# Performance work log

Measured on AMD Instinct MI355X. Metric: run time of the kernel, lower is better.

The kernel has to match this reference:

```python
import jax, jax.numpy as jnp
import numpy as np

N_HEADS = 2


def setup_inputs() -> dict:
    key = jax.random.key(0)
    ks = jax.random.split(key, 12)
    B, S, d, g = 4096, 32, 512, 512
    sp = (1.0 / np.sqrt(d))
    sg = (1.0 / np.sqrt(g))
    return {
        "source": jax.random.normal(ks[0], (B, d), jnp.float32),
        "gene": jax.random.normal(ks[1], (B, S, g), jnp.float32),
        "neighbors_padding_mask": jax.random.bernoulli(ks[2], 0.3, (B, S)),
        "mask_n": jax.random.uniform(ks[3], (B, 1), jnp.float32),
        "Wq": jax.random.normal(ks[4], (d, d), jnp.float32) * sp,
        "bq": jax.random.normal(ks[5], (d,), jnp.float32) * 0.02,
        "Wk": jax.random.normal(ks[6], (d, g), jnp.float32) * sg,
        "bk": jax.random.normal(ks[7], (d,), jnp.float32) * 0.02,
        "Wv": jax.random.normal(ks[8], (d, g), jnp.float32) * sg,
        "bv": jax.random.normal(ks[9], (d,), jnp.float32) * 0.02,
        "Wout": jax.random.normal(ks[10], (d, d), jnp.float32) * sp,
        "bout": jax.random.normal(ks[11], (d,), jnp.float32) * 0.02,
    }


def reference(source, gene, neighbors_padding_mask, mask_n,
              Wq, bq, Wk, bk, Wv, bv, Wout, bout):
    # attention_node.forward: 1-query masked MHA over S temporal neighbors.
    B, S, _ = gene.shape
    d = source.shape[1]
    H = N_HEADS
    hd = d // H

    # rows where every neighbor is padded -> unmask slot 0 (torch in-place fix)
    invalid = jnp.all(neighbors_padding_mask, axis=1, keepdims=True)      # [B,1]
    mask = neighbors_padding_mask.at[:, 0].set(
        jnp.where(invalid[:, 0], False, neighbors_padding_mask[:, 0]))

    # separate q/k/v projections (kdim=vdim=n_gene != embed_dim)
    q = (source @ Wq.T + bq) * (hd ** -0.5)                               # [B,d]
    k = gene @ Wk.T + bk                                                  # [B,S,d]
    v = gene @ Wv.T + bv                                                  # [B,S,d]

    qh = q.reshape(B, H, hd)
    kh = k.reshape(B, S, H, hd)
    vh = v.reshape(B, S, H, hd)

    scores = jnp.einsum('bhd,bshd->bhs', qh, kh)                          # [B,H,S]
    scores = jnp.where(mask[:, None, :], -jnp.inf, scores)
    w = jax.nn.softmax(scores, axis=-1)                                   # [B,H,S]

    attn = jnp.einsum('bhs,bshd->bhd', w, vh).reshape(B, d)               # [B,d]
    attn_out = attn @ Wout.T + bout

    # zero rows with no valid neighbors, gate, residual
    attn_out = jnp.where(invalid, jnp.float32(0), attn_out)
    out = attn_out * mask_n + source                                      # [B,d]
    attn_weight = w.mean(axis=1)                                          # avg over heads, [B,S]
    return out, attn_weight
```

## Files before the change

### kernel.cpp

```cpp
#include <hip/hip_runtime.h>
#include <hip/hip_bf16.h>
#include <math.h>
#include <stdint.h>


#define NB 4096
#define SNB 32
#define DM 512

typedef __attribute__((ext_vector_type(8))) short bf16x8;
typedef __attribute__((ext_vector_type(4))) float f32x4;

__device__ __forceinline__ unsigned short f2bf(float f) {
    union { float f; unsigned int u; } v; v.f = f;
    unsigned int u = v.u;
    return (unsigned short)((u + 0x7FFFu + ((u >> 16) & 1u)) >> 16);
}
__device__ __forceinline__ float bf2f(unsigned short s) {
    union { unsigned int u; float f; } v; v.u = ((unsigned int)s) << 16;
    return v.f;
}

__global__ __launch_bounds__(256) void k_prep(
    const float* __restrict__ src, const float* __restrict__ Wq,
    const float* __restrict__ bq, const float* __restrict__ Wk,
    const float* __restrict__ Wv, const float* __restrict__ Wout,
    const float* __restrict__ bv, const float* __restrict__ bout,
    const unsigned int* __restrict__ maskw,
    unsigned short* __restrict__ srcb, unsigned short* __restrict__ WkT,
    unsigned short* __restrict__ WqT, unsigned short* __restrict__ WvT,
    unsigned short* __restrict__ WoutB,
    float* __restrict__ cb, float* __restrict__ e, int* __restrict__ mode)
{
    __shared__ float tile[32][33];
    __shared__ int fF, fH;
    int bid = blockIdx.x, t = threadIdx.x;

    if (bid == 0) {
        if (t == 0) { fF = 0; fH = 0; }
        __syncthreads();
        int lf = 0, lh = 0;
        for (int i = t; i < 32768; i += 256) {
            unsigned int w = maskw[i];
            lf |= (w == 0x3F800000u);
            lh |= ((w & 0xFFFFFF00u) != 0u);
        }
        if (lf) atomicOr(&fF, 1);
        if (lh) atomicOr(&fH, 1);
        __syncthreads();
        if (t == 0) *mode = fF ? 2 : (fH ? 1 : 0);
        return;
    }
    if (bid <= 4) {
        int idx = (bid - 1) * 256 + t;
        int h = idx >> 9, j = idx & 511;
        float a = 0.f;
        for (int i = 0; i < 256; i++)
            a += Wk[(size_t)(h * 256 + i) * 512 + j] * bq[h * 256 + i];
        cb[idx] = 0.0625f * a;
        return;
    }
    if (bid <= 6) {
        int n = (bid - 5) * 256 + t;
        const float4* wr = (const float4*)(Wout + (size_t)n * 512);
        const float4* bv4 = (const float4*)bv;
        float a = bout[n];
        for (int q = 0; q < 128; q++) {
            float4 wv = wr[q], vv = bv4[q];
            a += wv.x * vv.x + wv.y * vv.y + wv.z * vv.z + wv.w * vv.w;
        }
        e[n] = a;
        return;
    }
    if (bid < 775) {
        const float* sm; unsigned short* dst; float scale; int tt;
        if (bid < 263)      { tt = bid - 7;   sm = Wk; dst = WkT; scale = 0.0625f; }
        else if (bid < 519) { tt = bid - 263; sm = Wv; dst = WvT; scale = 1.0f; }
        else                { tt = bid - 519; sm = Wq; dst = WqT; scale = 1.0f; }
        int i0 = (tt >> 4) << 5, j0 = (tt & 15) << 5;
        int r = t >> 3, c4 = (t & 7) << 2;
        float4 v = *(const float4*)(sm + (size_t)(i0 + r) * 512 + j0 + c4);
        tile[r][c4 + 0] = v.x; tile[r][c4 + 1] = v.y;
        tile[r][c4 + 2] = v.z; tile[r][c4 + 3] = v.w;
        __syncthreads();
        int jj = t >> 3, ig = (t & 7) << 2;
        int h = i0 >> 8, ib = i0 & 255;
        ushort4 o;
        o.x = f2bf(tile[ig + 0][jj] * scale);
        o.y = f2bf(tile[ig + 1][jj] * scale);
        o.z = f2bf(tile[ig + 2][jj] * scale);
        o.w = f2bf(tile[ig + 3][jj] * scale);
        *(ushort4*)(dst + (size_t)h * 131072 + (size_t)(j0 + jj) * 256 + ib + ig) = o;
        return;
    }
    if (bid < 807) {
        int base = (bid - 775) * 2048;
        for (int q = 0; q < 8; q++) {
            int idx = base + q * 256 + t;
            float4 v = ((const float4*)Wout)[idx];
            ushort4 o;
            o.x = f2bf(v.x); o.y = f2bf(v.y); o.z = f2bf(v.z); o.w = f2bf(v.w);
            ((ushort4*)WoutB)[idx] = o;
        }
        return;
    }
    {
        int base = (bid - 807) * 2048;
        for (int q = 0; q < 8; q++) {
            int idx = base + q * 256 + t;
            float4 v = ((const float4*)src)[idx];
            ushort4 o;
            o.x = f2bf(v.x); o.y = f2bf(v.y); o.z = f2bf(v.z); o.w = f2bf(v.w);
            ((ushort4*)srcb)[idx] = o;
        }
    }
}

__global__ __launch_bounds__(256) void k_cd(
    const unsigned short* __restrict__ WkT, const unsigned short* __restrict__ WqT,
    const unsigned short* __restrict__ WoutB, const unsigned short* __restrict__ WvT,
    unsigned short* __restrict__ C, unsigned short* __restrict__ D)
{
    __shared__ __align__(16) unsigned short As[64 * 40];
    __shared__ __align__(16) unsigned short Bs[64 * 40];
    int bid = blockIdx.x, t = threadIdx.x;
    const unsigned short *A, *Bt;
    unsigned short* outp;
    int lda, ldb, ldo;
    if (bid < 128) {
        int m0 = (bid >> 3) << 6, n0 = (bid & 7) << 6, h = m0 >> 9;
        A = WkT + (size_t)m0 * 256; lda = 256;
        Bt = WqT + (size_t)h * 131072 + (size_t)n0 * 256; ldb = 256;
        outp = C + (size_t)m0 * 512 + n0; ldo = 512;
    } else {
        int b2 = bid - 128;
        int m0 = (b2 >> 4) << 6, n0 = (b2 & 15) << 6, h = n0 >> 9;
        A = WoutB + (size_t)m0 * 512 + h * 256; lda = 512;
        Bt = WvT + (size_t)n0 * 256; ldb = 256;
        outp = D + (size_t)m0 * 1024 + n0; ldo = 1024;
    }
    int w = t >> 6, l = t & 63;
    int wm = (w >> 1) << 5, wn = (w & 1) << 5;
    int quad = l >> 4, lm = l & 15;
    f32x4 acc00 = {0.f,0.f,0.f,0.f}, acc01 = {0.f,0.f,0.f,0.f};
    f32x4 acc10 = {0.f,0.f,0.f,0.f}, acc11 = {0.f,0.f,0.f,0.f};
    int srow = t >> 2, spart = t & 3;
    const unsigned short* ag = A + (size_t)srow * lda + spart * 8;
    const unsigned short* bg = Bt + (size_t)srow * ldb + spart * 8;
    unsigned short* asl = As + srow * 40 + spart * 8;
    unsigned short* bsl = Bs + srow * 40 + spart * 8;
    for (int k0 = 0; k0 < 256; k0 += 32) {
        *(bf16x8*)asl = *(const bf16x8*)ag;
        *(bf16x8*)bsl = *(const bf16x8*)bg;
        ag += 32; bg += 32;
        __syncthreads();
        bf16x8 a0 = *(const bf16x8*)(As + (wm + lm) * 40 + quad * 8);
        bf16x8 a1 = *(const bf16x8*)(As + (wm + 16 + lm) * 40 + quad * 8);
        bf16x8 b0 = *(const bf16x8*)(Bs + (wn + lm) * 40 + quad * 8);
        bf16x8 b1 = *(const bf16x8*)(Bs + (wn + 16 + lm) * 40 + quad * 8);
        acc00 = __builtin_amdgcn_mfma_f32_16x16x32_bf16(a0, b0, acc00, 0, 0, 0);
        acc01 = __builtin_amdgcn_mfma_f32_16x16x32_bf16(a0, b1, acc01, 0, 0, 0);
        acc10 = __builtin_amdgcn_mfma_f32_16x16x32_bf16(a1, b0, acc10, 0, 0, 0);
        acc11 = __builtin_amdgcn_mfma_f32_16x16x32_bf16(a1, b1, acc11, 0, 0, 0);
        __syncthreads();
    }
    f32x4 accs[2][2] = {{acc00, acc01}, {acc10, acc11}};
    for (int ms = 0; ms < 2; ms++)
        for (int ns = 0; ns < 2; ns++)
            for (int r = 0; r < 4; r++)
                outp[(size_t)(wm + ms * 16 + quad * 4 + r) * ldo + wn + ns * 16 + lm] =
                    f2bf(accs[ms][ns][r]);
}

template <int EPI>
__global__ __launch_bounds__(256) void k_gemm_bt(
    const unsigned short* __restrict__ A, const unsigned short* __restrict__ Bt,
    void* __restrict__ outp, const float* __restrict__ bias,
    const float* __restrict__ gscale, const float* __restrict__ resid,
    int M, int N, int K)
{
    __shared__ __align__(16) unsigned short As[64 * 40];
    __shared__ __align__(16) unsigned short Bs[64 * 40];
    int nt = N >> 6;
    int m0 = ((int)blockIdx.x / nt) << 6;
    int n0 = ((int)blockIdx.x % nt) << 6;
    int t = threadIdx.x;
    int w = t >> 6, l = t & 63;
    int wm = (w >> 1) << 5, wn = (w & 1) << 5;
    int quad = l >> 4, lm = l & 15;

    f32x4 acc00 = {0.f,0.f,0.f,0.f}, acc01 = {0.f,0.f,0.f,0.f};
    f32x4 acc10 = {0.f,0.f,0.f,0.f}, acc11 = {0.f,0.f,0.f,0.f};

    int srow = t >> 2, spart = t & 3;
    const unsigned short* ag = A + (size_t)(m0 + srow) * K + spart * 8;
    const unsigned short* bg = Bt + (size_t)(n0 + srow) * K + spart * 8;
    unsigned short* asl = As + srow * 40 + spart * 8;
    unsigned short* bsl = Bs + srow * 40 + spart * 8;

    for (int k0 = 0; k0 < K; k0 += 32) {
        *(bf16x8*)asl = *(const bf16x8*)ag;
        *(bf16x8*)bsl = *(const bf16x8*)bg;
        ag += 32; bg += 32;
        __syncthreads();
        bf16x8 a0 = *(const bf16x8*)(As + (wm + lm) * 40 + quad * 8);
        bf16x8 a1 = *(const bf16x8*)(As + (wm + 16 + lm) * 40 + quad * 8);
        bf16x8 b0 = *(const bf16x8*)(Bs + (wn + lm) * 40 + quad * 8);
        bf16x8 b1 = *(const bf16x8*)(Bs + (wn + 16 + lm) * 40 + quad * 8);
        acc00 = __builtin_amdgcn_mfma_f32_16x16x32_bf16(a0, b0, acc00, 0, 0, 0);
        acc01 = __builtin_amdgcn_mfma_f32_16x16x32_bf16(a0, b1, acc01, 0, 0, 0);
        acc10 = __builtin_amdgcn_mfma_f32_16x16x32_bf16(a1, b0, acc10, 0, 0, 0);
        acc11 = __builtin_amdgcn_mfma_f32_16x16x32_bf16(a1, b1, acc11, 0, 0, 0);
        __syncthreads();
    }
    f32x4 accs[2][2] = {{acc00, acc01}, {acc10, acc11}};
    for (int ms = 0; ms < 2; ms++) {
        for (int ns = 0; ns < 2; ns++) {
            int n = n0 + wn + ns * 16 + lm;
            float bval = bias[n];
            for (int r = 0; r < 4; r++) {
                int m = m0 + wm + ms * 16 + quad * 4 + r;
                float v = accs[ms][ns][r] + bval;
                if (EPI == 0) {
                    ((unsigned short*)outp)[(size_t)m * N + n] = f2bf(v);
                } else {
                    ((float*)outp)[(size_t)m * N + n] =
                        v * gscale[m] + resid[(size_t)m * N + n];
                }
            }
        }
    }
}

__global__ __launch_bounds__(256) void k_attn(
    const float* __restrict__ gene, const unsigned short* __restrict__ QKb,
    const void* __restrict__ maskbuf, const int* __restrict__ modep,
    const float* __restrict__ mask_n,
    unsigned short* __restrict__ G, float* __restrict__ gscale,
    float* __restrict__ aw_out)
{
    __shared__ __align__(16) unsigned short glb[32 * 520];
    __shared__ __align__(16) float sp[4 * 64];
    __shared__ __align__(16) float wls[64];
    __shared__ int msk_s[32];

    int b = blockIdx.x, t = threadIdx.x;
    int w = t >> 6, l = t & 63, quad = l >> 4, lm = l & 15;

    bf16x8 af[4];
    {
        const unsigned short* qp = QKb + (size_t)b * 1024 + (size_t)lm * 512
                                 + w * 128 + quad * 8;
#pragma unroll
        for (int kk = 0; kk < 4; kk++) {
            bf16x8 z = {0,0,0,0,0,0,0,0};
            af[kk] = (lm < 2) ? *(const bf16x8*)(qp + kk * 32) : z;
        }
    }

    const float4* gp = (const float4*)(gene + (size_t)b * (SNB * DM));
    for (int it = 0; it < 8; it++) {
        float4 v0 = gp[t * 2 + it * 512];
        float4 v1 = gp[t * 2 + 1 + it * 512];
        int s = (t >> 6) + it * 4;
        int col = (t & 63) * 8;
        bf16x8 pk;
        pk[0] = (short)f2bf(v0.x); pk[1] = (short)f2bf(v0.y);
        pk[2] = (short)f2bf(v0.z); pk[3] = (short)f2bf(v0.w);
        pk[4] = (short)f2bf(v1.x); pk[5] = (short)f2bf(v1.y);
        pk[6] = (short)f2bf(v1.z); pk[7] = (short)f2bf(v1.w);
        *(bf16x8*)(glb + s * 520 + col) = pk;
    }
    int mode = *modep;
    if (t < 32) {
        size_t moff = (size_t)b * 32 + t;
        int mv;
        if (mode == 1)      mv = ((const unsigned char*)maskbuf)[moff] != 0;
        else if (mode == 2) mv = (((const float*)maskbuf)[moff] != 0.0f);
        else                mv = (((const int*)maskbuf)[moff] != 0);
        msk_s[t] = mv;
    }
    __syncthreads();

    if (t == 0) {
        int all = 1;
        for (int s = 0; s < 32; s++) all &= msk_s[s];
        if (all) msk_s[0] = 0;
        gscale[b] = all ? 0.0f : mask_n[b];
    }

    {
        f32x4 s0 = {0.f,0.f,0.f,0.f}, s1 = {0.f,0.f,0.f,0.f};
        int kb = w * 128;
#pragma unroll
        for (int kk = 0; kk < 4; kk++) {
            int k0 = kb + kk * 32;
            bf16x8 b0 = *(const bf16x8*)(glb + lm * 520 + k0 + quad * 8);
            bf16x8 b1 = *(const bf16x8*)(glb + (16 + lm) * 520 + k0 + quad * 8);
            s0 = __builtin_amdgcn_mfma_f32_16x16x32_bf16(af[kk], b0, s0, 0, 0, 0);
            s1 = __builtin_amdgcn_mfma_f32_16x16x32_bf16(af[kk], b1, s1, 0, 0, 0);
        }
        if (quad == 0) {
            sp[w * 64 + lm] = s0[0];
            sp[w * 64 + 32 + lm] = s0[1];
            sp[w * 64 + 16 + lm] = s1[0];
            sp[w * 64 + 48 + lm] = s1[1];
        }
    }
    __syncthreads();

    if (t < 64) {
        int s = t & 31;
        float v = sp[t] + sp[64 + t] + sp[128 + t] + sp[192 + t];
        int mk = msk_s[s];
        float vm = mk ? -1e30f : v;
        for (int off = 16; off > 0; off >>= 1) vm = fmaxf(vm, __shfl_xor(vm, off, 64));
        float ex = mk ? 0.0f : __expf(v - vm);
        float sm = ex;
        for (int off = 16; off > 0; off >>= 1) sm += __shfl_xor(sm, off, 64);
        wls[t] = ex / sm;
    }
    __syncthreads();

    if (t < 32) aw_out[(size_t)b * 32 + t] = 0.5f * (wls[t] + wls[32 + t]);

    {
        int h = t >> 7, jg = (t & 127) << 2;
        float a0 = 0.f, a1 = 0.f, a2 = 0.f, a3 = 0.f;
        const float* wrow = wls + h * 32;
        for (int s4 = 0; s4 < 8; s4++) {
            float4 wv = *(const float4*)(wrow + s4 * 4);
#pragma unroll
            for (int si = 0; si < 4; si++) {
                int s = s4 * 4 + si;
                ushort4 gv = *(const ushort4*)(glb + s * 520 + jg);
                float wq = (si == 0) ? wv.x : (si == 1) ? wv.y : (si == 2) ? wv.z : wv.w;
                a0 += wq * bf2f(gv.x); a1 += wq * bf2f(gv.y);
                a2 += wq * bf2f(gv.z); a3 += wq * bf2f(gv.w);
            }
        }
        ushort4 ov;
        ov.x = f2bf(a0); ov.y = f2bf(a1); ov.z = f2bf(a2); ov.w = f2bf(a3);
        *(ushort4*)(G + (size_t)b * 1024 + h * 512 + jg) = ov;
    }
}

extern "C" void kernel_launch(void* const* d_in, const int* in_sizes, int n_in,
                              void* d_out, int out_size, void* d_ws, size_t ws_size,
                              hipStream_t stream)
{
    const float* src   = (const float*)d_in[0];
    const float* gene  = (const float*)d_in[1];
    const void*  mask  = d_in[2];
    const float* maskn = (const float*)d_in[3];
    const float* Wq    = (const float*)d_in[4];
    const float* bq    = (const float*)d_in[5];
    const float* Wk    = (const float*)d_in[6];
    const float* Wv    = (const float*)d_in[8];
    const float* bv    = (const float*)d_in[9];
    const float* Wout  = (const float*)d_in[10];
    const float* bout  = (const float*)d_in[11];

    float* out = (float*)d_out;
    float* aw  = out + (size_t)NB * DM;

    char* ws = (char*)d_ws;
    size_t off = 0;
    auto alloc = [&](size_t bytes) -> void* {
        void* p = ws + off;
        off = (off + bytes + 255) & ~((size_t)255);
        return p;
    };
    int* mode            = (int*)alloc(4);
    unsigned short* srcb = (unsigned short*)alloc((size_t)NB * DM * 2);
    unsigned short* WkT  = (unsigned short*)alloc((size_t)1024 * 256 * 2);
    unsigned short* WqT  = (unsigned short*)alloc((size_t)1024 * 256 * 2);
    unsigned short* WvT  = (unsigned short*)alloc((size_t)1024 * 256 * 2);
    unsigned short* WoB  = (unsigned short*)alloc((size_t)512 * 512 * 2);
    unsigned short* Cb   = (unsigned short*)alloc((size_t)1024 * 512 * 2);
    unsigned short* Db   = (unsigned short*)alloc((size_t)512 * 1024 * 2);
    float* cb            = (float*)alloc(1024 * 4);
    float* ev            = (float*)alloc(512 * 4);
    unsigned short* QKb  = (unsigned short*)alloc((size_t)NB * 1024 * 2);
    unsigned short* G    = (unsigned short*)alloc((size_t)NB * 1024 * 2);
    float* gs            = (float*)alloc((size_t)NB * 4);

    k_prep<<<1063, 256, 0, stream>>>(src, Wq, bq, Wk, Wv, Wout, bv, bout,
                                     (const unsigned int*)mask,
                                     srcb, WkT, WqT, WvT, WoB, cb, ev, mode);
    k_cd<<<256, 256, 0, stream>>>(WkT, WqT, WoB, WvT, Cb, Db);
    k_gemm_bt<0><<<(4096 / 64) * (1024 / 64), 256, 0, stream>>>(
        srcb, Cb, QKb, cb, nullptr, nullptr, 4096, 1024, 512);
    k_attn<<<NB, 256, 0, stream>>>(gene, QKb, mask, mode, maskn, G, gs, aw);
    k_gemm_bt<1><<<(4096 / 64) * (512 / 64), 256, 0, stream>>>(
        G, Db, out, ev, gs, src, 4096, 512, 1024);
}
```

Measured before the change: 461.4 us.

## Fuse weight transpose/convert into C/D GEMMs and deepen GEMM k-step

Merges the prep kernel and the weight-product kernel so the C and D product GEMMs read fp32 weights directly, transposing and converting to bf16 on the fly into shared memory. This drops the intermediate WkT/WqT/WvT/WoutB buffers and one kernel launch. Separately, the main GEMM now stages 64 k-elements per barrier pair instead of 32, halving the number of synchronizations. The risks are strided scalar fp32 loads in the fused weight GEMMs, and the srcb conversion blocks running alongside the GEMM blocks in the same launch.

```diff
diff --git a/kernel.cpp b/kernel.cpp
--- a/kernel.cpp
+++ b/kernel.cpp
@@ -21,18 +21,18 @@
     return v.f;
 }
 
-__global__ __launch_bounds__(256) void k_prep(
+__global__ __launch_bounds__(256) void k_prep_cd(
     const float* __restrict__ src, const float* __restrict__ Wq,
     const float* __restrict__ bq, const float* __restrict__ Wk,
     const float* __restrict__ Wv, const float* __restrict__ Wout,
     const float* __restrict__ bv, const float* __restrict__ bout,
     const unsigned int* __restrict__ maskw,
-    unsigned short* __restrict__ srcb, unsigned short* __restrict__ WkT,
-    unsigned short* __restrict__ WqT, unsigned short* __restrict__ WvT,
-    unsigned short* __restrict__ WoutB,
-    float* __restrict__ cb, float* __restrict__ e, int* __restrict__ mode)
+    unsigned short* __restrict__ srcb, float* __restrict__ cb,
+    float* __restrict__ e, int* __restrict__ mode,
+    unsigned short* __restrict__ C, unsigned short* __restrict__ D)
 {
-    __shared__ float tile[32][33];
+    __shared__ __align__(16) unsigned short As[64 * 40];
+    __shared__ __align__(16) unsigned short Bs[64 * 40];
     __shared__ int fF, fH;
     int bid = blockIdx.x, t = threadIdx.x;
 
@@ -72,40 +72,8 @@
         e[n] = a;
         return;
     }
-    if (bid < 775) {
-        const float* sm; unsigned short* dst; float scale; int tt;
-        if (bid < 263)      { tt = bid - 7;   sm = Wk; dst = WkT; scale = 0.0625f; }
-        else if (bid < 519) { tt = bid - 263; sm = Wv; dst = WvT; scale = 1.0f; }
-        else                { tt = bid - 519; sm = Wq; dst = WqT; scale = 1.0f; }
-        int i0 = (tt >> 4) << 5, j0 = (tt & 15) << 5;
-        int r = t >> 3, c4 = (t & 7) << 2;
-        float4 v = *(const float4*)(sm + (size_t)(i0 + r) * 512 + j0 + c4);
-        tile[r][c4 + 0] = v.x; tile[r][c4 + 1] = v.y;
-        tile[r][c4 + 2] = v.z; tile[r][c4 + 3] = v.w;
-        __syncthreads();
-        int jj = t >> 3, ig = (t & 7) << 2;
-        int h = i0 >> 8, ib = i0 & 255;
-        ushort4 o;
-        o.x = f2bf(tile[ig + 0][jj] * scale);
-        o.y = f2bf(tile[ig + 1][jj] * scale);
-        o.z = f2bf(tile[ig + 2][jj] * scale);
-        o.w = f2bf(tile[ig + 3][jj] * scale);
-        *(ushort4*)(dst + (size_t)h * 131072 + (size_t)(j0 + jj) * 256 + ib + ig) = o;
-        return;
-    }
-    if (bid < 807) {
-        int base = (bid - 775) * 2048;
-        for (int q = 0; q < 8; q++) {
-            int idx = base + q * 256 + t;
-            float4 v = ((const float4*)Wout)[idx];
-            ushort4 o;
-            o.x = f2bf(v.x); o.y = f2bf(v.y); o.z = f2bf(v.z); o.w = f2bf(v.w);
-            ((ushort4*)WoutB)[idx] = o;
-        }
-        return;
-    }
-    {
-        int base = (bid - 807) * 2048;
+    if (bid < 263) {
+        int base = (bid - 7) * 2048;
         for (int q = 0; q < 8; q++) {
             int idx = base + q * 256 + t;
             float4 v = ((const float4*)src)[idx];
@@ -113,56 +81,80 @@
             o.x = f2bf(v.x); o.y = f2bf(v.y); o.z = f2bf(v.z); o.w = f2bf(v.w);
             ((ushort4*)srcb)[idx] = o;
         }
-    }
-}
-
-__global__ __launch_bounds__(256) void k_cd(
-    const unsigned short* __restrict__ WkT, const unsigned short* __restrict__ WqT,
-    const unsigned short* __restrict__ WoutB, const unsigned short* __restrict__ WvT,
-    unsigned short* __restrict__ C, unsigned short* __restrict__ D)
-{
-    __shared__ __align__(16) unsigned short As[64 * 40];
-    __shared__ __align__(16) unsigned short Bs[64 * 40];
-    int bid = blockIdx.x, t = threadIdx.x;
-    const unsigned short *A, *Bt;
-    unsigned short* outp;
-    int lda, ldb, ldo;
-    if (bid < 128) {
-        int m0 = (bid >> 3) << 6, n0 = (bid & 7) << 6, h = m0 >> 9;
-        A = WkT + (size_t)m0 * 256; lda = 256;
-        Bt = WqT + (size_t)h * 131072 + (size_t)n0 * 256; ldb = 256;
-        outp = C + (size_t)m0 * 512 + n0; ldo = 512;
-    } else {
-        int b2 = bid - 128;
-        int m0 = (b2 >> 4) << 6, n0 = (b2 & 15) << 6, h = n0 >> 9;
-        A = WoutB + (size_t)m0 * 512 + h * 256; lda = 512;
-        Bt = WvT + (size_t)n0 * 256; ldb = 256;
-        outp = D + (size_t)m0 * 1024 + n0; ldo = 1024;
-    }
+        return;
+    }
+
     int w = t >> 6, l = t & 63;
     int wm = (w >> 1) << 5, wn = (w & 1) << 5;
     int quad = l >> 4, lm = l & 15;
+    int sj = t & 63, si8 = (t >> 6) << 3;
     f32x4 acc00 = {0.f,0.f,0.f,0.f}, acc01 = {0.f,0.f,0.f,0.f};
     f32x4 acc10 = {0.f,0.f,0.f,0.f}, acc11 = {0.f,0.f,0.f,0.f};
-    int srow = t >> 2, spart = t & 3;
-    const unsigned short* ag = A + (size_t)srow * lda + spart * 8;
-    const unsigned short* bg = Bt + (size_t)srow * ldb + spart * 8;
-    unsigned short* asl = As + srow * 40 + spart * 8;
-    unsigned short* bsl = Bs + srow * 40 + spart * 8;
-    for (int k0 = 0; k0 < 256; k0 += 32) {
-        *(bf16x8*)asl = *(const bf16x8*)ag;
-        *(bf16x8*)bsl = *(const bf16x8*)bg;
-        ag += 32; bg += 32;
-        __syncthreads();
-        bf16x8 a0 = *(const bf16x8*)(As + (wm + lm) * 40 + quad * 8);
-        bf16x8 a1 = *(const bf16x8*)(As + (wm + 16 + lm) * 40 + quad * 8);
-        bf16x8 b0 = *(const bf16x8*)(Bs + (wn + lm) * 40 + quad * 8);
-        bf16x8 b1 = *(const bf16x8*)(Bs + (wn + 16 + lm) * 40 + quad * 8);
-        acc00 = __builtin_amdgcn_mfma_f32_16x16x32_bf16(a0, b0, acc00, 0, 0, 0);
-        acc01 = __builtin_amdgcn_mfma_f32_16x16x32_bf16(a0, b1, acc01, 0, 0, 0);
-        acc10 = __builtin_amdgcn_mfma_f32_16x16x32_bf16(a1, b0, acc10, 0, 0, 0);
-        acc11 = __builtin_amdgcn_mfma_f32_16x16x32_bf16(a1, b1, acc11, 0, 0, 0);
-        __syncthreads();
+
+    unsigned short* outp;
+    int ldo;
+    if (bid < 391) {
+        int tt = bid - 263;
+        int j0 = (tt >> 3) << 6, m0 = (tt & 7) << 6;
+        int jc = j0 & 511;
+        int ib = (j0 >> 9) << 8;
+        for (int ic = 0; ic < 8; ic++) {
+            int i0 = ib + ic * 32;
+            bf16x8 av, bw;
+#pragma unroll
+            for (int q = 0; q < 8; q++) {
+                av[q] = (short)f2bf(Wk[(size_t)(i0 + si8 + q) * 512 + jc + sj] * 0.0625f);
+                bw[q] = (short)f2bf(Wq[(size_t)(i0 + si8 + q) * 512 + m0 + sj]);
+            }
+            *(bf16x8*)(As + sj * 40 + si8) = av;
+            *(bf16x8*)(Bs + sj * 40 + si8) = bw;
+            __syncthreads();
+            bf16x8 a0 = *(const bf16x8*)(As + (wm + lm) * 40 + quad * 8);
+            bf16x8 a1 = *(const bf16x8*)(As + (wm + 16 + lm) * 40 + quad * 8);
+            bf16x8 b0 = *(const bf16x8*)(Bs + (wn + lm) * 40 + quad * 8);
+            bf16x8 b1 = *(const bf16x8*)(Bs + (wn + 16 + lm) * 40 + quad * 8);
+            acc00 = __builtin_amdgcn_mfma_f32_16x16x32_bf16(a0, b0, acc00, 0, 0, 0);
+            acc01 = __builtin_amdgcn_mfma_f32_16x16x32_bf16(a0, b1, acc01, 0, 0, 0);
+            acc10 = __builtin_amdgcn_mfma_f32_16x16x32_bf16(a1, b0, acc10, 0, 0, 0);
+            acc11 = __builtin_amdgcn_mfma_f32_16x16x32_bf16(a1, b1, acc11, 0, 0, 0);
+            __syncthreads();
+        }
+        outp = C + (size_t)j0 * 512 + m0; ldo = 512;
+    } else {
+        int tt = bid - 391;
+        int n0 = (tt >> 4) << 6, jh0 = (tt & 15) << 6;
+        int jc0 = jh0 & 511;
+        int ib = (jh0 >> 9) << 8;
+        int ra = t >> 2, ca = (t & 3) << 3;
+        for (int ic = 0; ic < 8; ic++) {
+            int i0 = ib + ic * 32;
+            {
+                const float4* p = (const float4*)(Wout + (size_t)(n0 + ra) * 512 + i0 + ca);
+                float4 v0 = p[0], v1 = p[1];
+                bf16x8 av;
+                av[0] = (short)f2bf(v0.x); av[1] = (short)f2bf(v0.y);
+                av[2] = (short)f2bf(v0.z); av[3] = (short)f2bf(v0.w);
+                av[4] = (short)f2bf(v1.x); av[5] = (short)f2bf(v1.y);
+                av[6] = (short)f2bf(v1.z); av[7] = (short)f2bf(v1.w);
+                *(bf16x8*)(As + ra * 40 + ca) = av;
+            }
+            bf16x8 bw;
+#pragma unroll
+            for (int q = 0; q < 8; q++)
+                bw[q] = (short)f2bf(Wv[(size_t)(i0 + si8 + q) * 512 + jc0 + sj]);
+            *(bf16x8*)(Bs + sj * 40 + si8) = bw;
+            __syncthreads();
+            bf16x8 a0 = *(const bf16x8*)(As + (wm + lm) * 40 + quad * 8);
+            bf16x8 a1 = *(const bf16x8*)(As + (wm + 16 + lm) * 40 + quad * 8);
+            bf16x8 b0 = *(const bf16x8*)(Bs + (wn + lm) * 40 + quad * 8);
+            bf16x8 b1 = *(const bf16x8*)(Bs + (wn + 16 + lm) * 40 + quad * 8);
+            acc00 = __builtin_amdgcn_mfma_f32_16x16x32_bf16(a0, b0, acc00, 0, 0, 0);
+            acc01 = __builtin_amdgcn_mfma_f32_16x16x32_bf16(a0, b1, acc01, 0, 0, 0);
+            acc10 = __builtin_amdgcn_mfma_f32_16x16x32_bf16(a1, b0, acc10, 0, 0, 0);
+            acc11 = __builtin_amdgcn_mfma_f32_16x16x32_bf16(a1, b1, acc11, 0, 0, 0);
+            __syncthreads();
+        }
+        outp = D + (size_t)n0 * 1024 + jh0; ldo = 1024;
     }
     f32x4 accs[2][2] = {{acc00, acc01}, {acc10, acc11}};
     for (int ms = 0; ms < 2; ms++)
@@ -179,8 +171,8 @@
     const float* __restrict__ gscale, const float* __restrict__ resid,
     int M, int N, int K)
 {
-    __shared__ __align__(16) unsigned short As[64 * 40];
-    __shared__ __align__(16) unsigned short Bs[64 * 40];
+    __shared__ __align__(16) unsigned short As[2][64 * 40];
+    __shared__ __align__(16) unsigned short Bs[2][64 * 40];
     int nt = N >> 6;
     int m0 = ((int)blockIdx.x / nt) << 6;
     int n0 = ((int)blockIdx.x % nt) << 6;
@@ -193,24 +185,30 @@
     f32x4 acc10 = {0.f,0.f,0.f,0.f}, acc11 = {0.f,0.f,0.f,0.f};
 
     int srow = t >> 2, spart = t & 3;
-    const unsigned short* ag = A + (size_t)(m0 + srow) * K + spart * 8;
-    const unsigned short* bg = Bt + (size_t)(n0 + srow) * K + spart * 8;
-    unsigned short* asl = As + srow * 40 + spart * 8;
-    unsigned short* bsl = Bs + srow * 40 + spart * 8;
-
-    for (int k0 = 0; k0 < K; k0 += 32) {
-        *(bf16x8*)asl = *(const bf16x8*)ag;
-        *(bf16x8*)bsl = *(const bf16x8*)bg;
-        ag += 32; bg += 32;
+    int chunk = spart >> 1, coff = (spart & 1) << 4;
+    const unsigned short* ag = A + (size_t)(m0 + srow) * K + spart * 16;
+    const unsigned short* bg = Bt + (size_t)(n0 + srow) * K + spart * 16;
+    unsigned short* asl = &As[chunk][srow * 40 + coff];
+    unsigned short* bsl = &Bs[chunk][srow * 40 + coff];
+
+    for (int k0 = 0; k0 < K; k0 += 64) {
+        *(bf16x8*)asl       = *(const bf16x8*)ag;
+        *(bf16x8*)(asl + 8) = *(const bf16x8*)(ag + 8);
+        *(bf16x8*)bsl       = *(const bf16x8*)bg;
+        *(bf16x8*)(bsl + 8) = *(const bf16x8*)(bg + 8);
+        ag += 64; bg += 64;
         __syncthreads();
-        bf16x8 a0 = *(const bf16x8*)(As + (wm + lm) * 40 + quad * 8);
-        bf16x8 a1 = *(const bf16x8*)(As + (wm + 16 + lm) * 40 + quad * 8);
-        bf16x8 b0 = *(const bf16x8*)(Bs + (wn + lm) * 40 + quad * 8);
-        bf16x8 b1 = *(const bf16x8*)(Bs + (wn + 16 + lm) * 40 + quad * 8);
-        acc00 = __builtin_amdgcn_mfma_f32_16x16x32_bf16(a0, b0, acc00, 0, 0, 0);
-        acc01 = __builtin_amdgcn_mfma_f32_16x16x32_bf16(a0, b1, acc01, 0, 0, 0);
-        acc10 = __builtin_amdgcn_mfma_f32_16x16x32_bf16(a1, b0, acc10, 0, 0, 0);
-        acc11 = __builtin_amdgcn_mfma_f32_16x16x32_bf16(a1, b1, acc11, 0, 0, 0);
+#pragma unroll
+        for (int c = 0; c < 2; c++) {
+            bf16x8 a0 = *(const bf16x8*)(&As[c][(wm + lm) * 40 + quad * 8]);
+            bf16x8 a1 = *(const bf16x8*)(&As[c][(wm + 16 + lm) * 40 + quad * 8]);
+            bf16x8 b0 = *(const bf16x8*)(&Bs[c][(wn + lm) * 40 + quad * 8]);
+            bf16x8 b1 = *(const bf16x8*)(&Bs[c][(wn + 16 + lm) * 40 + quad * 8]);
+            acc00 = __builtin_amdgcn_mfma_f32_16x16x32_bf16(a0, b0, acc00, 0, 0, 0);
+            acc01 = __builtin_amdgcn_mfma_f32_16x16x32_bf16(a0, b1, acc01, 0, 0, 0);
+            acc10 = __builtin_amdgcn_mfma_f32_16x16x32_bf16(a1, b0, acc10, 0, 0, 0);
+            acc11 = __builtin_amdgcn_mfma_f32_16x16x32_bf16(a1, b1, acc11, 0, 0, 0);
+        }
         __syncthreads();
     }
     f32x4 accs[2][2] = {{acc00, acc01}, {acc10, acc11}};
@@ -373,10 +371,6 @@
     };
     int* mode            = (int*)alloc(4);
     unsigned short* srcb = (unsigned short*)alloc((size_t)NB * DM * 2);
-    unsigned short* WkT  = (unsigned short*)alloc((size_t)1024 * 256 * 2);
-    unsigned short* WqT  = (unsigned short*)alloc((size_t)1024 * 256 * 2);
-    unsigned short* WvT  = (unsigned short*)alloc((size_t)1024 * 256 * 2);
-    unsigned short* WoB  = (unsigned short*)alloc((size_t)512 * 512 * 2);
     unsigned short* Cb   = (unsigned short*)alloc((size_t)1024 * 512 * 2);
     unsigned short* Db   = (unsigned short*)alloc((size_t)512 * 1024 * 2);
     float* cb            = (float*)alloc(1024 * 4);
@@ -385,10 +379,9 @@
     unsigned short* G    = (unsigned short*)alloc((size_t)NB * 1024 * 2);
     float* gs            = (float*)alloc((size_t)NB * 4);
 
-    k_prep<<<1063, 256, 0, stream>>>(src, Wq, bq, Wk, Wv, Wout, bv, bout,
-                                     (const unsigned int*)mask,
-                                     srcb, WkT, WqT, WvT, WoB, cb, ev, mode);
-    k_cd<<<256, 256, 0, stream>>>(WkT, WqT, WoB, WvT, Cb, Db);
+    k_prep_cd<<<519, 256, 0, stream>>>(src, Wq, bq, Wk, Wv, Wout, bv, bout,
+                                       (const unsigned int*)mask,
+                                       srcb, cb, ev, mode, Cb, Db);
     k_gemm_bt<0><<<(4096 / 64) * (1024 / 64), 256, 0, stream>>>(
         srcb, Cb, QKb, cb, nullptr, nullptr, 4096, 1024, 512);
     k_attn<<<NB, 256, 0, stream>>>(gene, QKb, mask, mode, maskn, G, gs, aw);
```

Result: faster. 450.8 us (-2.3%).
